# Kernel tuning notes

Measured on AMD Instinct MI355X. Metric: run time of the kernel, lower is better.

Reference implementation:

```python
import jax, jax.numpy as jnp
import numpy as np
from jax import lax

# SoftDTW constants from module-level `sdtw = SoftDTW(use_cuda=False, gamma=0.01, warp=134.4)`
GAMMA = 0.01
WARP = 134.4
BIG = 1e9        # finite stand-in for inf boundary (grad-safe; exp(-BIG/GAMMA) underflows to exactly 0)
MASK_INF = 100000.0
# loss alphas (config.loss.*)
KL_ALPHA = 1.0
KL_FWD_ALPHA = 1.0
GEN_ALPHA = 1.0
GEN_E2E_ALPHA = 1.0
FEAT_ALPHA = 2.0
DUR_ALPHA = 1.0
PITCH_ALPHA = 1.0
MEL_ALPHA = 45.0


def soft_dtw(D):
    """Soft-DTW with warp penalty (NaturalSpeech variant).
    D: [b, n, m] cost matrix. Returns [b] soft-DTW values R[n-1, m-1] of
      R[i,j] = D[i,j] + softmin_gamma(R[i-1,j-1], R[i-1,j]+warp, R[i,j-1]+warp)
    computed over anti-diagonals (wavefront) so each scan step is vectorized.
    """
    b, n, m = D.shape
    K = n + m - 1
    i_idx = jnp.arange(n)
    ks = jnp.arange(K)

    def pack(k):  # pack anti-diagonal k of D, indexed by row i
        j = k - i_idx
        v = (j >= 0) & (j < m)
        return jnp.where(v[None, :], D[:, i_idx, jnp.clip(j, 0, m - 1)], 0.0), v

    Dd, Vd = jax.vmap(pack)(ks)  # Dd: [K, b, n], Vd: [K, n]
    init = jnp.full((b, n), BIG, dtype=D.dtype)

    def step(carry, xs):
        r1, r2 = carry  # previous diag (k-1) and diag (k-2), indexed by row i
        dk, v, k = xs
        # diagonal predecessor (i-1, j-1): on diag k-2 at row i-1; (−1,−1) boundary = 0 only at k==0
        first = jnp.where(k == 0, 0.0, BIG).astype(D.dtype)
        r_diag = jnp.concatenate([jnp.broadcast_to(first, (b, 1)), r2[:, :-1]], axis=1)
        # up predecessor (i-1, j): diag k-1, row i-1
        r_up = jnp.concatenate([jnp.full((b, 1), BIG, dtype=D.dtype), r1[:, :-1]], axis=1)
        # left predecessor (i, j-1): diag k-1, row i
        stacked = jnp.stack([-r_diag, -(r_up + WARP), -(r1 + WARP)]) / GAMMA
        smin = -GAMMA * jax.nn.logsumexp(stacked, axis=0)
        r_new = jnp.where(v[None, :], dk + smin, BIG)
        return (r_new, r1), None

    (rf, _), _ = lax.scan(step, (init, init), (Dd, Vd, ks))
    return rf[:, n - 1]  # cell (n-1, m-1) lies on the last diagonal at row n-1


def kl_matrix(z, lq, m, lp):
    """kl[b,p,q] = sum_h lp - lq - 0.5 + 0.5*(z-m)^2*exp(-2lp); rows (m,lp) [b,h,P], cols (z,lq) [b,h,Q]."""
    h = m.shape[1]
    a = jnp.exp(-2.0 * lp)  # [b,h,P]
    quad = (jnp.einsum('bhp,bhq->bpq', a, z * z)
            - 2.0 * jnp.einsum('bhp,bhq->bpq', a * m, z)
            + jnp.sum(a * m * m, axis=1)[:, :, None])
    return jnp.sum(lp, axis=1)[:, :, None] - jnp.sum(lq, axis=1)[:, None, :] - 0.5 * h + 0.5 * quad


def kl_loss_sdtw(z, lq, m, lp, p_mask, q_mask):
    kl = kl_matrix(z, lq, m, lp)
    kl = jnp.pad(kl, ((0, 0), (0, 1), (0, 1)))
    pmf = jnp.pad(p_mask.astype(jnp.float32), ((0, 0), (0, 1)))
    qmf = jnp.pad(q_mask.astype(jnp.float32), ((0, 0), (0, 1)))
    pb, qb = pmf.astype(bool), qmf.astype(bool)
    kl = jnp.where(pb[:, :, None] ^ qb[:, None, :], MASK_INF, kl)
    kl = jnp.where((~pb[:, :, None]) & (~qb[:, None, :]), 0.0, kl)
    return soft_dtw(kl).sum() / pmf.sum()


def setup_inputs() -> dict:
    key = jax.random.key(0)
    ks = jax.random.split(key, 16)
    B, H, T = 8, 192, 400
    d = {
        'mel_slice': jax.random.normal(ks[0], (B, 80, T), jnp.float32),
        'mel_slice_hat': jax.random.normal(ks[1], (B, 80, T), jnp.float32),
        'scores_disc_fake': jax.random.normal(ks[2], (6, B, T), jnp.float32),
        'scores_disc_fake_e2e': jax.random.normal(ks[3], (6, B, T), jnp.float32),
        'feats_disc_real': jax.random.normal(ks[4], (30, B, 128, T), jnp.float32),
        'feats_disc_fake': jax.random.normal(ks[5], (30, B, 128, T), jnp.float32),
        'duration_loss': jax.random.uniform(ks[6], (1,), jnp.float32),
        'pitch_loss': jax.random.uniform(ks[7], (1,), jnp.float32),
        'z_p': jax.random.normal(ks[8], (B, H, T), jnp.float32),
        'm_p': jax.random.normal(ks[9], (B, H, T), jnp.float32),
        'logs_p': jax.random.normal(ks[10], (B, H, T), jnp.float32),
        'z_q': jax.random.normal(ks[11], (B, H, T), jnp.float32),
        'm_q': jax.random.normal(ks[12], (B, H, T), jnp.float32),
        'logs_q': jax.random.normal(ks[13], (B, H, T), jnp.float32),
        'p_mask': jnp.ones((B, T), jnp.int32),
        'z_mask': jnp.ones((B, T), jnp.int32),
    }
    return d


def reference(mel_slice, mel_slice_hat, scores_disc_fake, scores_disc_fake_e2e,
              feats_disc_real, feats_disc_fake, duration_loss, pitch_loss,
              z_p, m_p, logs_p, z_q, m_q, logs_q, p_mask, z_mask):
    # generator losses: sum over discriminator maps of mean((1 - s)^2)
    loss_gen = jnp.mean((1.0 - scores_disc_fake) ** 2, axis=(1, 2)).sum() * GEN_ALPHA
    loss_gen_e2e = jnp.mean((1.0 - scores_disc_fake_e2e) ** 2, axis=(1, 2)).sum() * GEN_E2E_ALPHA
    # feature matching: 2 * sum over feature maps of mean|real.detach() - fake|
    fr = lax.stop_gradient(feats_disc_real)
    loss_fm = 2.0 * jnp.mean(jnp.abs(fr - feats_disc_fake), axis=(1, 2, 3)).sum() * FEAT_ALPHA
    loss_mel = jnp.mean(jnp.abs(mel_slice - mel_slice_hat)) * MEL_ALPHA
    loss_dur = jnp.sum(duration_loss) * DUR_ALPHA
    loss_pitch = jnp.sum(pitch_loss) * PITCH_ALPHA
    # soft-DTW KL (both directions)
    loss_kl = kl_loss_sdtw(z_p, logs_q, m_p, logs_p, p_mask, z_mask) * KL_ALPHA
    loss_kl_fwd = kl_loss_sdtw(z_q, logs_p, m_q, logs_q, z_mask, p_mask) * KL_FWD_ALPHA
    total = loss_gen + loss_gen_e2e + loss_fm + loss_mel + loss_dur + loss_pitch + loss_kl + loss_kl_fwd
    return jnp.stack([loss_gen, loss_gen_e2e, loss_fm, loss_mel, loss_dur,
                      loss_pitch, loss_kl, loss_kl_fwd, total])
```

## Files before the change

kernel.cpp:

```cpp
#include <hip/hip_runtime.h>
#include <math.h>

#define BIGV      1e9f
#define WARP_PEN  134.4f
#define MASK_INF_C 100000.0f

#define B   8
#define H   192
#define T   400
#define NP  401
#define NPROB 16
#define TSLAB 166464
#define SBLOCKS 768
#define KLBLOCKS (49 * NPROB)

typedef float f32x4 __attribute__((ext_vector_type(4)));

#define SLOT_OFF 16
#define LSP_OFF 160
#define LSQ_OFF (160 + B*T)
#define C1P_OFF (160 + 2*B*T)
#define C1Q_OFF (160 + 3*B*T)
#define DMAT_OFF (160 + 4*B*T)

__device__ __forceinline__ int diag_len(int s) { return (s <= 50) ? s + 1 : 101 - s; }
__device__ __forceinline__ int diag_i0 (int s) { return (s <= 50) ? 0 : s - 50; }
__device__ __forceinline__ int diag_Cs (int s) {
    return (s <= 51) ? s * (s + 1) / 2 : 2601 - (101 - s) * (102 - s) / 2;
}

__device__ __forceinline__ float wave_shr1(float src, float fill) {
    int r = __builtin_amdgcn_update_dpp(__float_as_int(fill), __float_as_int(src),
                                        0x138 , 0xf, 0xf, false);
    return __int_as_float(r);
}

__global__ __launch_bounds__(256)
void colsum(const float* __restrict__ logs_p, const float* __restrict__ m_p,
            const float* __restrict__ logs_q, const float* __restrict__ m_q,
            float* __restrict__ ws) {
    int b = blockIdx.x / 7;
    int lane = threadIdx.x & 63;
    int hq = threadIdx.x >> 6;
    int t = (blockIdx.x % 7) * 64 + lane;
    __shared__ float part[4][4][64];
    float lp_s = 0.f, lq_s = 0.f, c1p = 0.f, c1q = 0.f;
    if (t < T) {
        int base = b*H*T + hq*48*T + t;
        const float* LP = logs_p + base;
        const float* MP = m_p   + base;
        const float* LQ = logs_q + base;
        const float* MQ = m_q   + base;
#pragma unroll 4
        for (int h = 0; h < 48; ++h) {
            float lp = LP[h*T], mp = MP[h*T];
            float lq = LQ[h*T], mq = MQ[h*T];
            lp_s += lp;
            lq_s += lq;
            c1p += __expf(-2.f*lp) * mp * mp;
            c1q += __expf(-2.f*lq) * mq * mq;
        }
    }
    part[hq][0][lane] = lp_s;
    part[hq][1][lane] = lq_s;
    part[hq][2][lane] = c1p;
    part[hq][3][lane] = c1q;
    __syncthreads();
    if (hq == 0 && t < T) {
        float a0 = part[0][0][lane] + part[1][0][lane] + part[2][0][lane] + part[3][0][lane];
        float a1 = part[0][1][lane] + part[1][1][lane] + part[2][1][lane] + part[3][1][lane];
        float a2 = part[0][2][lane] + part[1][2][lane] + part[2][2][lane] + part[3][2][lane];
        float a3 = part[0][3][lane] + part[1][3][lane] + part[2][3][lane] + part[3][3][lane];
        ws[LSP_OFF + b*T + t] = a0;
        ws[LSQ_OFF + b*T + t] = a1;
        ws[C1P_OFF + b*T + t] = a2;
        ws[C1Q_OFF + b*T + t] = a3;
    }
}

#define TILE 64
#define KH 32
__global__ __launch_bounds__(256)
void fused_kl_scalar(const float* __restrict__ z_p, const float* __restrict__ m_p,
                     const float* __restrict__ logs_p,
                     const float* __restrict__ z_q, const float* __restrict__ m_q,
                     const float* __restrict__ logs_q,
                     const int* __restrict__ p_mask, const int* __restrict__ z_mask,
                     float* __restrict__ ws,
                     const float* __restrict__ mel, const float* __restrict__ melh,
                     const float* __restrict__ sg,  const float* __restrict__ se,
                     const float* __restrict__ fr,  const float* __restrict__ ff) {
    __shared__ __align__(16) float As [KH][TILE+4];
    __shared__ __align__(16) float AMs[KH][TILE+4];
    __shared__ __align__(16) float Zs [KH][TILE+4];
    __shared__ __align__(16) float Z2s[KH][TILE+4];
    __shared__ float red[4][8];

    if (blockIdx.x < KLBLOCKS) {
        int prob = blockIdx.x / 49;
        int bx   = blockIdx.x % 49;
        int dir = prob >> 3, b = prob & 7;
        int tp = bx / 7, tq = bx % 7;
        int p0 = tp * TILE, q0 = tq * TILE;

        const float* lp_arr = dir ? logs_q : logs_p;
        const float* m_arr  = dir ? m_q    : m_p;
        const float* z_arr  = dir ? z_q    : z_p;
        const float* Lp = ws + (dir ? LSQ_OFF : LSP_OFF) + b*T;
        const float* Lq = ws + (dir ? LSP_OFF : LSQ_OFF) + b*T;
        const float* C1 = ws + (dir ? C1Q_OFF : C1P_OFF) + b*T;
        const int* rmask = dir ? z_mask : p_mask;
        const int* cmask = dir ? p_mask : z_mask;

        int tid = threadIdx.x;
        int tx = tid & 15, ty = tid >> 4;

        float acc1[4][4] = {{0.f}}, acc2[4][4] = {{0.f}};

        const float* lpB = lp_arr + b*H*T;
        const float* mB  = m_arr  + b*H*T;
        const float* zB  = z_arr  + b*H*T;

        for (int h0 = 0; h0 < H; h0 += KH) {
            for (int e = tid; e < KH*TILE; e += 256) {
                int hh = e >> 6, tt = e & 63;
                int pg = p0 + tt; if (pg > T-1) pg = T-1;
                int qg = q0 + tt; if (qg > T-1) qg = T-1;
                float lp = lpB[(h0+hh)*T + pg];
                float mv = mB [(h0+hh)*T + pg];
                float a  = __expf(-2.f*lp);
                As [hh][tt] = a;
                AMs[hh][tt] = a * mv;
                float zv = zB[(h0+hh)*T + qg];
                Zs [hh][tt] = zv;
                Z2s[hh][tt] = zv * zv;
            }
            __syncthreads();
#pragma unroll 8
            for (int hh = 0; hh < KH; ++hh) {
                const float4 av  = *(const float4*)(&As [hh][ty*4]);
                const float4 amv = *(const float4*)(&AMs[hh][ty*4]);
                const float4 zv  = *(const float4*)(&Zs [hh][tx*4]);
                const float4 z2v = *(const float4*)(&Z2s[hh][tx*4]);
                const float pa[4]  = {av.x, av.y, av.z, av.w};
                const float pam[4] = {amv.x, amv.y, amv.z, amv.w};
                const float qz[4]  = {zv.x, zv.y, zv.z, zv.w};
                const float qz2[4] = {z2v.x, z2v.y, z2v.z, z2v.w};
#pragma unroll
                for (int ii = 0; ii < 4; ++ii)
#pragma unroll
                    for (int jj = 0; jj < 4; ++jj) {
                        acc1[ii][jj] = fmaf(pa[ii],  qz2[jj], acc1[ii][jj]);
                        acc2[ii][jj] = fmaf(pam[ii], qz[jj],  acc2[ii][jj]);
                    }
            }
            __syncthreads();
        }

        float* Dm = ws + DMAT_OFF + (size_t)prob * TSLAB;
#pragma unroll
        for (int ii = 0; ii < 4; ++ii) {
            int p = p0 + ty*4 + ii;
            if (p > NP-1) continue;
            int pc = p < T ? p : T-1;
            float lpv = Lp[pc];
            float c1v = C1[pc];
            bool pmv = (p < T) && (rmask[b*T + p] != 0);
#pragma unroll
            for (int jj = 0; jj < 4; ++jj) {
                int q = q0 + tx*4 + jj;
                if (q > NP-1) continue;
                int qc = q < T ? q : T-1;
                bool qmv = (q < T) && (cmask[b*T + q] != 0);
                float val = lpv - Lq[qc] - 0.5f*(float)H
                          + 0.5f*(acc1[ii][jj] - 2.f*acc2[ii][jj] + c1v);
                float outv = (pmv != qmv) ? MASK_INF_C : ((!pmv && !qmv) ? 0.f : val);
                int I8 = p >> 3, J8 = q >> 3, sdg = I8 + J8;
                int len = diag_len(sdg), i0 = diag_i0(sdg), Cs = diag_Cs(sdg);
                int k = (p & 7) * 2 + ((q & 7) >> 2);
                int off = Cs*64 + (k*len + (I8 - i0))*4 + (q & 3);
                Dm[off] = outv;
            }
        }
    } else {
        float s0 = 0.f, s1 = 0.f, s2 = 0.f, s3 = 0.f, s4 = 0.f, s5 = 0.f;
        int tid = (blockIdx.x - KLBLOCKS) * 256 + threadIdx.x;
        const int stride = SBLOCKS * 256;

        const float4* fr4 = (const float4*)fr;
        const float4* ff4 = (const float4*)ff;
        for (int i = tid; i < 3072000; i += stride) {
            float4 a = fr4[i], b = ff4[i];
            s2 += fabsf(a.x - b.x) + fabsf(a.y - b.y) + fabsf(a.z - b.z) + fabsf(a.w - b.w);
        }
        const float4* m4 = (const float4*)mel;
        const float4* mh4 = (const float4*)melh;
        for (int i = tid; i < 64000; i += stride) {
            float4 a = m4[i], b = mh4[i];
            s3 += fabsf(a.x - b.x) + fabsf(a.y - b.y) + fabsf(a.z - b.z) + fabsf(a.w - b.w);
        }
        const float4* g4 = (const float4*)sg;
        const float4* e4 = (const float4*)se;
        for (int i = tid; i < 4800; i += stride) {
            float4 a = g4[i], b = e4[i];
            float gx = 1.f - a.x, gy = 1.f - a.y, gz = 1.f - a.z, gw = 1.f - a.w;
            s0 += gx*gx + gy*gy + gz*gz + gw*gw;
            float hx = 1.f - b.x, hy = 1.f - b.y, hz = 1.f - b.z, hw = 1.f - b.w;
            s1 += hx*hx + hy*hy + hz*hz + hw*hw;
        }
        for (int i = tid; i < B*T; i += stride) {
            s4 += (float)p_mask[i];
            s5 += (float)z_mask[i];
        }
        for (int off = 32; off > 0; off >>= 1) {
            s0 += __shfl_down(s0, off); s1 += __shfl_down(s1, off);
            s2 += __shfl_down(s2, off); s3 += __shfl_down(s3, off);
            s4 += __shfl_down(s4, off); s5 += __shfl_down(s5, off);
        }
        int wid = threadIdx.x >> 6;
        if ((threadIdx.x & 63) == 0) {
            red[wid][0] = s0; red[wid][1] = s1; red[wid][2] = s2;
            red[wid][3] = s3; red[wid][4] = s4; red[wid][5] = s5;
        }
        __syncthreads();
        if (threadIdx.x == 0) {
            float t0 = 0.f, t1 = 0.f, t2 = 0.f, t3 = 0.f, t4 = 0.f, t5 = 0.f;
#pragma unroll
            for (int w = 0; w < 4; ++w) {
                t0 += red[w][0]; t1 += red[w][1]; t2 += red[w][2];
                t3 += red[w][3]; t4 += red[w][4]; t5 += red[w][5];
            }
            float* slot = ws + SLOT_OFF + (blockIdx.x & 7) * 16;
            atomicAdd(&slot[0], t0); atomicAdd(&slot[1], t1);
            atomicAdd(&slot[2], t2); atomicAdd(&slot[3], t3);
            atomicAdd(&slot[4], t4); atomicAdd(&slot[5], t5);
        }
    }
}

__global__ __launch_bounds__(64, 1)
void dtw_diag(const float* __restrict__ Dd, float* __restrict__ acc) {
    int prob = blockIdx.x;
    int lane = threadIdx.x;
    const float* Dp = Dd + (size_t)prob * TSLAB;

    float brow[8], browW[8], rightraw[8], rightW[8];
    float brold = BIGV, v00 = BIGV;
#pragma unroll
    for (int t = 0; t < 8; ++t) {
        brow[t] = BIGV; browW[t] = BIGV; rightraw[t] = BIGV; rightW[t] = BIGV;
    }

    f32x4 bufA[16], bufB[16], bufC[16];

    auto load_diag = [&](int sp, f32x4* buf) {
        if (sp > 100) sp = 100;
        int len = diag_len(sp), i0 = diag_i0(sp), Cs = diag_Cs(sp);
        int pos = lane - i0;
        pos = pos < 0 ? 0 : pos;
        pos = pos > len - 1 ? len - 1 : pos;
        const float* srcb = Dp + Cs*64 + pos*4;
        int str = len * 4;
#pragma unroll
        for (int k = 0; k < 16; ++k)
            buf[k] = *(const f32x4*)(srcb + k*str);
    };

#define TILE_STEP(CUR, NXT, SVAL, DO_LOAD)                                    \
    {                                                                          \
        const int s_ = (SVAL);                                                 \
        if (DO_LOAD) {                                                         \
            load_diag(s_ + 2, NXT);                                            \
            __builtin_amdgcn_sched_barrier(0);  \
        }                                                                      \
        bool jz = (s_ == lane);                                    \
        float brnew = brow[7];                                                 \
        _Pragma("unroll")                                                      \
        for (int c = 0; c < 8; ++c) {                                          \
            brow[c] = wave_shr1(brow[c], BIGV);                                \
            browW[c] = brow[c] + WARP_PEN;                                     \
        }                                                                      \
        float corner = wave_shr1(brold, BIGV);                                 \
        if (jz) corner = (lane == 0) ? 0.f : BIGV;                             \
        float dprev = corner;                                                  \
        _Pragma("unroll")                                                      \
        for (int r = 0; r < 8; ++r) {                                          \
            float leftW = jz ? BIGV : rightW[r];                               \
            float dnextrow = jz ? BIGV : rightraw[r];                          \
            float diag = dprev;                                                \
            _Pragma("unroll")                                                  \
            for (int ch = 0; ch < 2; ++ch) {                                   \
                f32x4 dvv = CUR[r*2 + ch];                                     \
                _Pragma("unroll")                                              \
                for (int cc = 0; cc < 4; ++cc) {                               \
                    const int c = ch*4 + cc;                                   \
                    float v = fminf(fminf(diag, browW[c]), leftW) + dvv[cc];   \
                    if (r == 0 && c == 0) v00 = v;                             \
                    float t_ = brow[c];                                        \
                    brow[c] = v;                                               \
                    float vW = v + WARP_PEN;                                   \
                    browW[c] = vW;                                             \
                    leftW = vW;                                                \
                    diag = t_;                                                 \
                }                                                              \
            }                                                                  \
            rightraw[r] = brow[7];                                             \
            rightW[r]   = browW[7];                                            \
            dprev = dnextrow;                                                  \
        }                                                                      \
        brold = brnew;                                                         \
    }

    load_diag(0, bufA);
    load_diag(1, bufB);

    for (int sb = 0; sb < 99; sb += 3) {
        TILE_STEP(bufA, bufC, sb,     1)
        TILE_STEP(bufB, bufA, sb + 1, 1)
        TILE_STEP(bufC, bufB, sb + 2, 1)
    }
    TILE_STEP(bufA, bufC, 99,  0)
    TILE_STEP(bufB, bufC, 100, 0)
#undef TILE_STEP

    if (lane == 50) atomicAdd(&acc[6 + (prob >> 3)], v00);
}

__global__ void finalize(const float* __restrict__ acc,
                         const float* __restrict__ dur,
                         const float* __restrict__ pit,
                         float* __restrict__ out) {
    if (threadIdx.x != 0 || blockIdx.x != 0) return;
    float t[6] = {0.f, 0.f, 0.f, 0.f, 0.f, 0.f};
    for (int s = 0; s < 8; ++s)
        for (int c = 0; c < 6; ++c)
            t[c] += acc[SLOT_OFF + s*16 + c];
    float gen  = t[0] / 3200.f;
    float e2e  = t[1] / 3200.f;
    float fm   = 4.f * t[2] / 409600.f;
    float melv = 45.f * t[3] / 256000.f;
    float d    = dur[0];
    float p    = pit[0];
    float kl   = acc[6] / t[4];
    float klf  = acc[7] / t[5];
    out[0] = gen; out[1] = e2e; out[2] = fm; out[3] = melv;
    out[4] = d;   out[5] = p;   out[6] = kl; out[7] = klf;
    out[8] = gen + e2e + fm + melv + d + p + kl + klf;
}

extern "C" void kernel_launch(void* const* d_in, const int* in_sizes, int n_in,
                              void* d_out, int out_size, void* d_ws, size_t ws_size,
                              hipStream_t stream) {
    const float* mel    = (const float*)d_in[0];
    const float* melh   = (const float*)d_in[1];
    const float* sg     = (const float*)d_in[2];
    const float* se     = (const float*)d_in[3];
    const float* fr     = (const float*)d_in[4];
    const float* ff     = (const float*)d_in[5];
    const float* dur    = (const float*)d_in[6];
    const float* pit    = (const float*)d_in[7];
    const float* z_p    = (const float*)d_in[8];
    const float* m_p    = (const float*)d_in[9];
    const float* logs_p = (const float*)d_in[10];
    const float* z_q    = (const float*)d_in[11];
    const float* m_q    = (const float*)d_in[12];
    const float* logs_q = (const float*)d_in[13];
    const int*   p_mask = (const int*)d_in[14];
    const int*   z_mask = (const int*)d_in[15];
    float* ws  = (float*)d_ws;
    float* out = (float*)d_out;

    hipMemsetAsync(ws, 0, 160 * sizeof(float), stream);
    colsum<<<B*7, 256, 0, stream>>>(logs_p, m_p, logs_q, m_q, ws);
    fused_kl_scalar<<<KLBLOCKS + SBLOCKS, 256, 0, stream>>>(
        z_p, m_p, logs_p, z_q, m_q, logs_q, p_mask, z_mask, ws,
        mel, melh, sg, se, fr, ff);
    dtw_diag<<<NPROB, 64, 0, stream>>>(ws + DMAT_OFF, ws);
    finalize<<<1, 64, 0, stream>>>(ws, dur, pit, out);
}
```

Before: 140.6 us.

## Fuse DTW wavefront into KL/reduction kernel with per-problem completion counters

Merges the soft-DTW kernel into the fused KL-matrix and scalar-reduction kernel. The first 16 blocks spin on a per-problem atomic counter until all 49 KL tiles for their problem have been written, then run the DTW scan, so DTW can start while other KL tiles and the large feature-matching reduction are still running. This removes one kernel launch and the serialization between the KL and DTW stages. It relies on the spinning blocks being co-resident with the producer blocks (they are placed first so producers can be scheduled), and the spinning DTW blocks hold CU slots and may compete with the bandwidth-bound reduction.

Measured after the change: 206.5 us (median of 2 runs). +46.9%, slower.

```diff
diff --git a/kernel.cpp b/kernel.cpp
--- a/kernel.cpp
+++ b/kernel.cpp
@@ -17,6 +17,7 @@
 typedef float f32x4 __attribute__((ext_vector_type(4)));
 
 #define SLOT_OFF 16
+#define CNT_OFF 128
 #define LSP_OFF 160
 #define LSQ_OFF (160 + B*T)
 #define C1P_OFF (160 + 2*B*T)
@@ -81,199 +82,62 @@
 #define TILE 64
 #define KH 32
 __global__ __launch_bounds__(256)
-void fused_kl_scalar(const float* __restrict__ z_p, const float* __restrict__ m_p,
-                     const float* __restrict__ logs_p,
-                     const float* __restrict__ z_q, const float* __restrict__ m_q,
-                     const float* __restrict__ logs_q,
-                     const int* __restrict__ p_mask, const int* __restrict__ z_mask,
-                     float* __restrict__ ws,
-                     const float* __restrict__ mel, const float* __restrict__ melh,
-                     const float* __restrict__ sg,  const float* __restrict__ se,
-                     const float* __restrict__ fr,  const float* __restrict__ ff) {
+void mega_fused(const float* __restrict__ z_p, const float* __restrict__ m_p,
+                const float* __restrict__ logs_p,
+                const float* __restrict__ z_q, const float* __restrict__ m_q,
+                const float* __restrict__ logs_q,
+                const int* __restrict__ p_mask, const int* __restrict__ z_mask,
+                float* __restrict__ ws,
+                const float* __restrict__ mel, const float* __restrict__ melh,
+                const float* __restrict__ sg,  const float* __restrict__ se,
+                const float* __restrict__ fr,  const float* __restrict__ ff) {
     __shared__ __align__(16) float As [KH][TILE+4];
     __shared__ __align__(16) float AMs[KH][TILE+4];
     __shared__ __align__(16) float Zs [KH][TILE+4];
     __shared__ __align__(16) float Z2s[KH][TILE+4];
     __shared__ float red[4][8];
-
-    if (blockIdx.x < KLBLOCKS) {
-        int prob = blockIdx.x / 49;
-        int bx   = blockIdx.x % 49;
-        int dir = prob >> 3, b = prob & 7;
-        int tp = bx / 7, tq = bx % 7;
-        int p0 = tp * TILE, q0 = tq * TILE;
-
-        const float* lp_arr = dir ? logs_q : logs_p;
-        const float* m_arr  = dir ? m_q    : m_p;
-        const float* z_arr  = dir ? z_q    : z_p;
-        const float* Lp = ws + (dir ? LSQ_OFF : LSP_OFF) + b*T;
-        const float* Lq = ws + (dir ? LSP_OFF : LSQ_OFF) + b*T;
-        const float* C1 = ws + (dir ? C1Q_OFF : C1P_OFF) + b*T;
-        const int* rmask = dir ? z_mask : p_mask;
-        const int* cmask = dir ? p_mask : z_mask;
-
-        int tid = threadIdx.x;
-        int tx = tid & 15, ty = tid >> 4;
-
-        float acc1[4][4] = {{0.f}}, acc2[4][4] = {{0.f}};
-
-        const float* lpB = lp_arr + b*H*T;
-        const float* mB  = m_arr  + b*H*T;
-        const float* zB  = z_arr  + b*H*T;
-
-        for (int h0 = 0; h0 < H; h0 += KH) {
-            for (int e = tid; e < KH*TILE; e += 256) {
-                int hh = e >> 6, tt = e & 63;
-                int pg = p0 + tt; if (pg > T-1) pg = T-1;
-                int qg = q0 + tt; if (qg > T-1) qg = T-1;
-                float lp = lpB[(h0+hh)*T + pg];
-                float mv = mB [(h0+hh)*T + pg];
-                float a  = __expf(-2.f*lp);
-                As [hh][tt] = a;
-                AMs[hh][tt] = a * mv;
-                float zv = zB[(h0+hh)*T + qg];
-                Zs [hh][tt] = zv;
-                Z2s[hh][tt] = zv * zv;
-            }
-            __syncthreads();
-#pragma unroll 8
-            for (int hh = 0; hh < KH; ++hh) {
-                const float4 av  = *(const float4*)(&As [hh][ty*4]);
-                const float4 amv = *(const float4*)(&AMs[hh][ty*4]);
-                const float4 zv  = *(const float4*)(&Zs [hh][tx*4]);
-                const float4 z2v = *(const float4*)(&Z2s[hh][tx*4]);
-                const float pa[4]  = {av.x, av.y, av.z, av.w};
-                const float pam[4] = {amv.x, amv.y, amv.z, amv.w};
-                const float qz[4]  = {zv.x, zv.y, zv.z, zv.w};
-                const float qz2[4] = {z2v.x, z2v.y, z2v.z, z2v.w};
-#pragma unroll
-                for (int ii = 0; ii < 4; ++ii)
-#pragma unroll
-                    for (int jj = 0; jj < 4; ++jj) {
-                        acc1[ii][jj] = fmaf(pa[ii],  qz2[jj], acc1[ii][jj]);
-                        acc2[ii][jj] = fmaf(pam[ii], qz[jj],  acc2[ii][jj]);
-                    }
-            }
-            __syncthreads();
-        }
-
-        float* Dm = ws + DMAT_OFF + (size_t)prob * TSLAB;
-#pragma unroll
-        for (int ii = 0; ii < 4; ++ii) {
-            int p = p0 + ty*4 + ii;
-            if (p > NP-1) continue;
-            int pc = p < T ? p : T-1;
-            float lpv = Lp[pc];
-            float c1v = C1[pc];
-            bool pmv = (p < T) && (rmask[b*T + p] != 0);
-#pragma unroll
-            for (int jj = 0; jj < 4; ++jj) {
-                int q = q0 + tx*4 + jj;
-                if (q > NP-1) continue;
-                int qc = q < T ? q : T-1;
-                bool qmv = (q < T) && (cmask[b*T + q] != 0);
-                float val = lpv - Lq[qc] - 0.5f*(float)H
-                          + 0.5f*(acc1[ii][jj] - 2.f*acc2[ii][jj] + c1v);
-                float outv = (pmv != qmv) ? MASK_INF_C : ((!pmv && !qmv) ? 0.f : val);
-                int I8 = p >> 3, J8 = q >> 3, sdg = I8 + J8;
-                int len = diag_len(sdg), i0 = diag_i0(sdg), Cs = diag_Cs(sdg);
-                int k = (p & 7) * 2 + ((q & 7) >> 2);
-                int off = Cs*64 + (k*len + (I8 - i0))*4 + (q & 3);
-                Dm[off] = outv;
-            }
-        }
-    } else {
-        float s0 = 0.f, s1 = 0.f, s2 = 0.f, s3 = 0.f, s4 = 0.f, s5 = 0.f;
-        int tid = (blockIdx.x - KLBLOCKS) * 256 + threadIdx.x;
-        const int stride = SBLOCKS * 256;
-
-        const float4* fr4 = (const float4*)fr;
-        const float4* ff4 = (const float4*)ff;
-        for (int i = tid; i < 3072000; i += stride) {
-            float4 a = fr4[i], b = ff4[i];
-            s2 += fabsf(a.x - b.x) + fabsf(a.y - b.y) + fabsf(a.z - b.z) + fabsf(a.w - b.w);
-        }
-        const float4* m4 = (const float4*)mel;
-        const float4* mh4 = (const float4*)melh;
-        for (int i = tid; i < 64000; i += stride) {
-            float4 a = m4[i], b = mh4[i];
-            s3 += fabsf(a.x - b.x) + fabsf(a.y - b.y) + fabsf(a.z - b.z) + fabsf(a.w - b.w);
-        }
-        const float4* g4 = (const float4*)sg;
-        const float4* e4 = (const float4*)se;
-        for (int i = tid; i < 4800; i += stride) {
-            float4 a = g4[i], b = e4[i];
-            float gx = 1.f - a.x, gy = 1.f - a.y, gz = 1.f - a.z, gw = 1.f - a.w;
-            s0 += gx*gx + gy*gy + gz*gz + gw*gw;
-            float hx = 1.f - b.x, hy = 1.f - b.y, hz = 1.f - b.z, hw = 1.f - b.w;
-            s1 += hx*hx + hy*hy + hz*hz + hw*hw;
-        }
-        for (int i = tid; i < B*T; i += stride) {
-            s4 += (float)p_mask[i];
-            s5 += (float)z_mask[i];
-        }
-        for (int off = 32; off > 0; off >>= 1) {
-            s0 += __shfl_down(s0, off); s1 += __shfl_down(s1, off);
-            s2 += __shfl_down(s2, off); s3 += __shfl_down(s3, off);
-            s4 += __shfl_down(s4, off); s5 += __shfl_down(s5, off);
-        }
-        int wid = threadIdx.x >> 6;
-        if ((threadIdx.x & 63) == 0) {
-            red[wid][0] = s0; red[wid][1] = s1; red[wid][2] = s2;
-            red[wid][3] = s3; red[wid][4] = s4; red[wid][5] = s5;
-        }
-        __syncthreads();
-        if (threadIdx.x == 0) {
-            float t0 = 0.f, t1 = 0.f, t2 = 0.f, t3 = 0.f, t4 = 0.f, t5 = 0.f;
-#pragma unroll
-            for (int w = 0; w < 4; ++w) {
-                t0 += red[w][0]; t1 += red[w][1]; t2 += red[w][2];
-                t3 += red[w][3]; t4 += red[w][4]; t5 += red[w][5];
-            }
-            float* slot = ws + SLOT_OFF + (blockIdx.x & 7) * 16;
-            atomicAdd(&slot[0], t0); atomicAdd(&slot[1], t1);
-            atomicAdd(&slot[2], t2); atomicAdd(&slot[3], t3);
-            atomicAdd(&slot[4], t4); atomicAdd(&slot[5], t5);
-        }
-    }
-}
-
-__global__ __launch_bounds__(64, 1)
-void dtw_diag(const float* __restrict__ Dd, float* __restrict__ acc) {
-    int prob = blockIdx.x;
-    int lane = threadIdx.x;
-    const float* Dp = Dd + (size_t)prob * TSLAB;
-
-    float brow[8], browW[8], rightraw[8], rightW[8];
-    float brold = BIGV, v00 = BIGV;
-#pragma unroll
-    for (int t = 0; t < 8; ++t) {
-        brow[t] = BIGV; browW[t] = BIGV; rightraw[t] = BIGV; rightW[t] = BIGV;
-    }
-
-    f32x4 bufA[16], bufB[16], bufC[16];
-
-    auto load_diag = [&](int sp, f32x4* buf) {
-        if (sp > 100) sp = 100;
-        int len = diag_len(sp), i0 = diag_i0(sp), Cs = diag_Cs(sp);
-        int pos = lane - i0;
-        pos = pos < 0 ? 0 : pos;
-        pos = pos > len - 1 ? len - 1 : pos;
-        const float* srcb = Dp + Cs*64 + pos*4;
-        int str = len * 4;
-#pragma unroll
-        for (int k = 0; k < 16; ++k)
-            buf[k] = *(const f32x4*)(srcb + k*str);
-    };
+    unsigned* cnt = (unsigned*)(ws + CNT_OFF);
+
+    if (blockIdx.x < NPROB) {
+        if (threadIdx.x >= 64) return;
+        int prob = blockIdx.x;
+        int lane = threadIdx.x;
+        const float* Dp = ws + DMAT_OFF + (size_t)prob * TSLAB;
+
+        while (__hip_atomic_load(&cnt[prob], __ATOMIC_ACQUIRE,
+                                 __HIP_MEMORY_SCOPE_AGENT) < 49u)
+            __builtin_amdgcn_s_sleep(8);
+
+        float brow[8], browW[8], rightraw[8], rightW[8];
+        float brold = BIGV, v00 = BIGV;
+#pragma unroll
+        for (int t = 0; t < 8; ++t) {
+            brow[t] = BIGV; browW[t] = BIGV; rightraw[t] = BIGV; rightW[t] = BIGV;
+        }
+
+        f32x4 bufA[16], bufB[16], bufC[16];
+
+        auto load_diag = [&](int sp, f32x4* buf) {
+            if (sp > 100) sp = 100;
+            int len = diag_len(sp), i0 = diag_i0(sp), Cs = diag_Cs(sp);
+            int pos = lane - i0;
+            pos = pos < 0 ? 0 : pos;
+            pos = pos > len - 1 ? len - 1 : pos;
+            const float* srcb = Dp + Cs*64 + pos*4;
+            int str = len * 4;
+#pragma unroll
+            for (int k = 0; k < 16; ++k)
+                buf[k] = *(const f32x4*)(srcb + k*str);
+        };
 
 #define TILE_STEP(CUR, NXT, SVAL, DO_LOAD)                                    \
     {                                                                          \
         const int s_ = (SVAL);                                                 \
         if (DO_LOAD) {                                                         \
             load_diag(s_ + 2, NXT);                                            \
-            __builtin_amdgcn_sched_barrier(0);  \
+            __builtin_amdgcn_sched_barrier(0);                                 \
         }                                                                      \
-        bool jz = (s_ == lane);                                    \
+        bool jz = (s_ == lane);                                                \
         float brnew = brow[7];                                                 \
         _Pragma("unroll")                                                      \
         for (int c = 0; c < 8; ++c) {                                          \
@@ -311,19 +175,165 @@
         brold = brnew;                                                         \
     }
 
-    load_diag(0, bufA);
-    load_diag(1, bufB);
-
-    for (int sb = 0; sb < 99; sb += 3) {
-        TILE_STEP(bufA, bufC, sb,     1)
-        TILE_STEP(bufB, bufA, sb + 1, 1)
-        TILE_STEP(bufC, bufB, sb + 2, 1)
+        load_diag(0, bufA);
+        load_diag(1, bufB);
+
+        for (int sb = 0; sb < 99; sb += 3) {
+            TILE_STEP(bufA, bufC, sb,     1)
+            TILE_STEP(bufB, bufA, sb + 1, 1)
+            TILE_STEP(bufC, bufB, sb + 2, 1)
+        }
+        TILE_STEP(bufA, bufC, 99,  0)
+        TILE_STEP(bufB, bufC, 100, 0)
+#undef TILE_STEP
+
+        if (lane == 50) atomicAdd(&ws[6 + (prob >> 3)], v00);
+    } else if (blockIdx.x < NPROB + KLBLOCKS) {
+        int kbx  = blockIdx.x - NPROB;
+        int prob = kbx / 49;
+        int bx   = kbx % 49;
+        int dir = prob >> 3, b = prob & 7;
+        int tp = bx / 7, tq = bx % 7;
+        int p0 = tp * TILE, q0 = tq * TILE;
+
+        const float* lp_arr = dir ? logs_q : logs_p;
+        const float* m_arr  = dir ? m_q    : m_p;
+        const float* z_arr  = dir ? z_q    : z_p;
+        const float* Lp = ws + (dir ? LSQ_OFF : LSP_OFF) + b*T;
+        const float* Lq = ws + (dir ? LSP_OFF : LSQ_OFF) + b*T;
+        const float* C1 = ws + (dir ? C1Q_OFF : C1P_OFF) + b*T;
+        const int* rmask = dir ? z_mask : p_mask;
+        const int* cmask = dir ? p_mask : z_mask;
+
+        int tid = threadIdx.x;
+        int tx = tid & 15, ty = tid >> 4;
+
+        float acc1[4][4] = {{0.f}}, acc2[4][4] = {{0.f}};
+
+        const float* lpB = lp_arr + b*H*T;
+        const float* mB  = m_arr  + b*H*T;
+        const float* zB  = z_arr  + b*H*T;
+
+        for (int h0 = 0; h0 < H; h0 += KH) {
+            for (int e = tid; e < KH*TILE; e += 256) {
+                int hh = e >> 6, tt = e & 63;
+                int pg = p0 + tt; if (pg > T-1) pg = T-1;
+                int qg = q0 + tt; if (qg > T-1) qg = T-1;
+                float lp = lpB[(h0+hh)*T + pg];
+                float mv = mB [(h0+hh)*T + pg];
+                float a  = __expf(-2.f*lp);
+                As [hh][tt] = a;
+                AMs[hh][tt] = a * mv;
+                float zv = zB[(h0+hh)*T + qg];
+                Zs [hh][tt] = zv;
+                Z2s[hh][tt] = zv * zv;
+            }
+            __syncthreads();
+#pragma unroll 8
+            for (int hh = 0; hh < KH; ++hh) {
+                const float4 av  = *(const float4*)(&As [hh][ty*4]);
+                const float4 amv = *(const float4*)(&AMs[hh][ty*4]);
+                const float4 zv  = *(const float4*)(&Zs [hh][tx*4]);
+                const float4 z2v = *(const float4*)(&Z2s[hh][tx*4]);
+                const float pa[4]  = {av.x, av.y, av.z, av.w};
+                const float pam[4] = {amv.x, amv.y, amv.z, amv.w};
+                const float qz[4]  = {zv.x, zv.y, zv.z, zv.w};
+                const float qz2[4] = {z2v.x, z2v.y, z2v.z, z2v.w};
+#pragma unroll
+                for (int ii = 0; ii < 4; ++ii)
+#pragma unroll
+                    for (int jj = 0; jj < 4; ++jj) {
+                        acc1[ii][jj] = fmaf(pa[ii],  qz2[jj], acc1[ii][jj]);
+                        acc2[ii][jj] = fmaf(pam[ii], qz[jj],  acc2[ii][jj]);
+                    }
+            }
+            __syncthreads();
+        }
+
+        float* Dm = ws + DMAT_OFF + (size_t)prob * TSLAB;
+#pragma unroll
+        for (int ii = 0; ii < 4; ++ii) {
+            int p = p0 + ty*4 + ii;
+            if (p <= NP-1) {
+                int pc = p < T ? p : T-1;
+                float lpv = Lp[pc];
+                float c1v = C1[pc];
+                bool pmv = (p < T) && (rmask[b*T + p] != 0);
+#pragma unroll
+                for (int jj = 0; jj < 4; ++jj) {
+                    int q = q0 + tx*4 + jj;
+                    if (q > NP-1) continue;
+                    int qc = q < T ? q : T-1;
+                    bool qmv = (q < T) && (cmask[b*T + q] != 0);
+                    float val = lpv - Lq[qc] - 0.5f*(float)H
+                              + 0.5f*(acc1[ii][jj] - 2.f*acc2[ii][jj] + c1v);
+                    float outv = (pmv != qmv) ? MASK_INF_C : ((!pmv && !qmv) ? 0.f : val);
+                    int I8 = p >> 3, J8 = q >> 3, sdg = I8 + J8;
+                    int len = diag_len(sdg), i0 = diag_i0(sdg), Cs = diag_Cs(sdg);
+                    int k = (p & 7) * 2 + ((q & 7) >> 2);
+                    int off = Cs*64 + (k*len + (I8 - i0))*4 + (q & 3);
+                    Dm[off] = outv;
+                }
+            }
+        }
+        __syncthreads();
+        if (threadIdx.x == 0)
+            __hip_atomic_fetch_add(&cnt[prob], 1u, __ATOMIC_RELEASE,
+                                   __HIP_MEMORY_SCOPE_AGENT);
+    } else {
+        float s0 = 0.f, s1 = 0.f, s2 = 0.f, s3 = 0.f, s4 = 0.f, s5 = 0.f;
+        int tid = (blockIdx.x - NPROB - KLBLOCKS) * 256 + threadIdx.x;
+        const int stride = SBLOCKS * 256;
+
+        const float4* fr4 = (const float4*)fr;
+        const float4* ff4 = (const float4*)ff;
+        for (int i = tid; i < 3072000; i += stride) {
+            float4 a = fr4[i], b = ff4[i];
+            s2 += fabsf(a.x - b.x) + fabsf(a.y - b.y) + fabsf(a.z - b.z) + fabsf(a.w - b.w);
+        }
+        const float4* m4 = (const float4*)mel;
+        const float4* mh4 = (const float4*)melh;
+        for (int i = tid; i < 64000; i += stride) {
+            float4 a = m4[i], b = mh4[i];
+            s3 += fabsf(a.x - b.x) + fabsf(a.y - b.y) + fabsf(a.z - b.z) + fabsf(a.w - b.w);
+        }
+        const float4* g4 = (const float4*)sg;
+        const float4* e4 = (const float4*)se;
+        for (int i = tid; i < 4800; i += stride) {
+            float4 a = g4[i], b = e4[i];
+            float gx = 1.f - a.x, gy = 1.f - a.y, gz = 1.f - a.z, gw = 1.f - a.w;
+            s0 += gx*gx + gy*gy + gz*gz + gw*gw;
+            float hx = 1.f - b.x, hy = 1.f - b.y, hz = 1.f - b.z, hw = 1.f - b.w;
+            s1 += hx*hx + hy*hy + hz*hz + hw*hw;
+        }
+        for (int i = tid; i < B*T; i += stride) {
+            s4 += (float)p_mask[i];
+            s5 += (float)z_mask[i];
+        }
+        for (int off = 32; off > 0; off >>= 1) {
+            s0 += __shfl_down(s0, off); s1 += __shfl_down(s1, off);
+            s2 += __shfl_down(s2, off); s3 += __shfl_down(s3, off);
+            s4 += __shfl_down(s4, off); s5 += __shfl_down(s5, off);
+        }
+        int wid = threadIdx.x >> 6;
+        if ((threadIdx.x & 63) == 0) {
+            red[wid][0] = s0; red[wid][1] = s1; red[wid][2] = s2;
+            red[wid][3] = s3; red[wid][4] = s4; red[wid][5] = s5;
+        }
+        __syncthreads();
+        if (threadIdx.x == 0) {
+            float t0 = 0.f, t1 = 0.f, t2 = 0.f, t3 = 0.f, t4 = 0.f, t5 = 0.f;
+#pragma unroll
+            for (int w = 0; w < 4; ++w) {
+                t0 += red[w][0]; t1 += red[w][1]; t2 += red[w][2];
+                t3 += red[w][3]; t4 += red[w][4]; t5 += red[w][5];
+            }
+            float* slot = ws + SLOT_OFF + (blockIdx.x & 7) * 16;
+            atomicAdd(&slot[0], t0); atomicAdd(&slot[1], t1);
+            atomicAdd(&slot[2], t2); atomicAdd(&slot[3], t3);
+            atomicAdd(&slot[4], t4); atomicAdd(&slot[5], t5);
+        }
     }
-    TILE_STEP(bufA, bufC, 99,  0)
-    TILE_STEP(bufB, bufC, 100, 0)
-#undef TILE_STEP
-
-    if (lane == 50) atomicAdd(&acc[6 + (prob >> 3)], v00);
 }
 
 __global__ void finalize(const float* __restrict__ acc,
@@ -372,9 +382,8 @@
 
     hipMemsetAsync(ws, 0, 160 * sizeof(float), stream);
     colsum<<<B*7, 256, 0, stream>>>(logs_p, m_p, logs_q, m_q, ws);
-    fused_kl_scalar<<<KLBLOCKS + SBLOCKS, 256, 0, stream>>>(
+    mega_fused<<<NPROB + KLBLOCKS + SBLOCKS, 256, 0, stream>>>(
         z_p, m_p, logs_p, z_q, m_q, logs_q, p_mask, z_mask, ws,
         mel, melh, sg, se, fr, ff);
-    dtw_diag<<<NPROB, 64, 0, stream>>>(ws + DMAT_OFF, ws);
     finalize<<<1, 64, 0, stream>>>(ws, dur, pit, out);
 }
```
